# Optimization experiments

Hardware: AMD Instinct MI355X
Metric: run time of the kernel (lower is better)

## Reference

```python
import jax, jax.numpy as jnp
import numpy as np


def setup_inputs() -> dict:
    key = jax.random.key(0)
    k1, k2 = jax.random.split(key)
    flow = jax.random.normal(k1, (4, 2, 256, 256), dtype=jnp.float32)   # [B,2,H,W] per-pixel flow over dt
    spike = jax.random.uniform(k2, (4, 64, 256, 256), dtype=jnp.float32)  # [B,C,H,W] spike voxel grid
    return {"flow": flow, "spike": spike}


def _splat(vals, xn, yn, H, W):
    """Forward bilinear splat of vals [H,W] to continuous coords (xn,yn) [H,W]."""
    x0 = jnp.floor(xn)
    y0 = jnp.floor(yn)
    wx = xn - x0  # fractional weights (differentiable w.r.t. flow)
    wy = yn - y0
    x0i = x0.astype(jnp.int32)
    y0i = y0.astype(jnp.int32)
    out = jnp.zeros(H * W, dtype=vals.dtype)
    corners = (
        (0, 0, (1.0 - wx) * (1.0 - wy)),
        (1, 0, wx * (1.0 - wy)),
        (0, 1, (1.0 - wx) * wy),
        (1, 1, wx * wy),
    )
    for dx, dy, w in corners:
        xi = x0i + dx
        yi = y0i + dy
        valid = (xi >= 0) & (xi < W) & (yi >= 0) & (yi < H)
        idx = jnp.clip(yi, 0, H - 1) * W + jnp.clip(xi, 0, W - 1)
        out = out.at[idx.ravel()].add(jnp.where(valid, w * vals, 0.0).ravel())
    return out.reshape(H, W)


def spike_warp_mid(spike, flow, dt):
    """Warp each time bin c by flow * (c - mid)/dt toward the middle timestamp (bilinear splat)."""
    B, C, H, W = spike.shape
    mid = (C - 1) / 2.0
    yy, xx = jnp.meshgrid(jnp.arange(H, dtype=spike.dtype),
                          jnp.arange(W, dtype=spike.dtype), indexing='ij')
    s = (jnp.arange(C, dtype=spike.dtype) - mid) / jnp.asarray(dt, spike.dtype)  # [C]
    u = flow[:, 0][:, None]  # [B,1,H,W]
    v = flow[:, 1][:, None]
    xn = xx + u * s[None, :, None, None]  # [B,C,H,W]
    yn = yy + v * s[None, :, None, None]
    splat_bc = jax.vmap(jax.vmap(lambda va, xa, ya: _splat(va, xa, ya, H, W)))
    return splat_bc(spike, xn, yn)  # [B,C,H,W]


def reference(flow, spike):
    B, C, H, W = spike.shape
    spike_warped = spike_warp_mid(spike, flow, dt=64)
    # Faithful to original: sum over BATCH dim inside per-batch loop (same each iter),
    # so loss = (B * -var) / B = -var(spike_image) with unbiased variance.
    spike_image = jnp.sum(spike_warped, axis=0)  # [C,H,W]
    loss = -jnp.var(spike_image - jnp.mean(spike_image), ddof=1)
    return loss
```

## Files before the change

### kernel.cpp

```cpp
#include <hip/hip_runtime.h>

typedef float f2 __attribute__((ext_vector_type(2)));

constexpr int B = 4, C = 64, H = 256, W = 256;
constexpr int HW = H * W;
constexpr long long N_TOT = (long long)C * HW;

constexpr int TS = 16;
constexpr int R = 4;
constexpr int SW = 24;
constexpr int SAREA = SW * SW;
constexpr int NBLK = 256 * 8;

__global__ __launch_bounds__(256) void fused_kernel(
    const float* __restrict__ flow,
    const float* __restrict__ spike,
    double* __restrict__ partials) {
  __shared__ f2 uv[SAREA];
  __shared__ f2 spk[SAREA * 4];
  __shared__ float wmx[4], wmy[4];
  __shared__ double red[8];

  const int bid = blockIdx.x;
  const int tile = bid & 255;
  const int j = bid >> 8;
  const int tx0 = (tile & 15) * TS;
  const int ty0 = (tile >> 4) * TS;
  const int tid = threadIdx.x;
  const int qx = tid & 15, qy = tid >> 4;
  const int wave = tid >> 6;

  f2 smv[4];
  float smag3;
#pragma unroll
  for (int t = 0; t < 4; ++t) {
    float sm = ((float)(4 * j + t) + 0.5f) * (1.0f / 64.0f);
    smv[t] = f2{-sm, sm};
    if (t == 3) smag3 = sm;
  }
  const int cn0 = 31 - 4 * j;
  const int cp0 = 32 + 4 * j;

  f2 acc2[4];
#pragma unroll
  for (int t = 0; t < 4; ++t) acc2[t] = f2{0.f, 0.f};

  bool c_act[3], c_val[3];
  int c_apos[3], c_gp[3];
#pragma unroll
  for (int k = 0; k < 3; ++k) {
    int pos = tid + 256 * k;
    c_act[k] = pos < SAREA;
    int row = pos / SW;
    int col = pos - row * SW;
    c_apos[k] = pos;
    int gy = ty0 + row - R, gx = tx0 + col - R;
    c_val[k] = c_act[k] & ((unsigned)gy < (unsigned)H) & ((unsigned)gx < (unsigned)W);
    c_gp[k] = gy * W + gx;
  }

  float p_u[3], p_v[3];
  float4 p_a[3], p_b[3];

  auto prefetch = [&](int b) {
    const float* fu = flow + (size_t)b * 2 * HW;
    const float* fv = fu + HW;
    const float* spb = spike + (size_t)b * C * HW;
#pragma unroll
    for (int k = 0; k < 3; ++k) {
      float u = 0.f, v = 0.f;
      float4 a = {0.f, 0.f, 0.f, 0.f};
      float4 d = {0.f, 0.f, 0.f, 0.f};
      if (c_val[k]) {
        int gp = c_gp[k];
        u = fu[gp];
        v = fv[gp];
        a.x = spb[(size_t)cn0 * HW + gp];
        a.y = spb[(size_t)(cn0 - 1) * HW + gp];
        a.z = spb[(size_t)(cn0 - 2) * HW + gp];
        a.w = spb[(size_t)(cn0 - 3) * HW + gp];
        d.x = spb[(size_t)cp0 * HW + gp];
        d.y = spb[(size_t)(cp0 + 1) * HW + gp];
        d.z = spb[(size_t)(cp0 + 2) * HW + gp];
        d.w = spb[(size_t)(cp0 + 3) * HW + gp];
      }
      p_u[k] = u; p_v[k] = v; p_a[k] = a; p_b[k] = d;
    }
  };

  prefetch(0);

  const int qpos = (qy + R) * SW + (qx + R);

  for (int b = 0; b < B; ++b) {
    float mu = 0.f, mv = 0.f;
#pragma unroll
    for (int k = 0; k < 3; ++k) {
      if (c_act[k]) {
        int ap = c_apos[k];
        uv[ap] = f2{p_u[k], p_v[k]};
        f2* sp = &spk[ap * 4];
        sp[0] = f2{p_a[k].x, p_b[k].x};
        sp[1] = f2{p_a[k].y, p_b[k].y};
        sp[2] = f2{p_a[k].z, p_b[k].z};
        sp[3] = f2{p_a[k].w, p_b[k].w};
        mu = fmaxf(mu, fabsf(p_u[k]));
        mv = fmaxf(mv, fabsf(p_v[k]));
      }
    }
    for (int off = 32; off > 0; off >>= 1) {
      mu = fmaxf(mu, __shfl_down(mu, off, 64));
      mv = fmaxf(mv, __shfl_down(mv, off, 64));
    }
    if ((tid & 63) == 0) { wmx[wave] = mu; wmy[wave] = mv; }
    __syncthreads();
    float bu = fmaxf(fmaxf(wmx[0], wmx[1]), fmaxf(wmx[2], wmx[3]));
    float bv = fmaxf(fmaxf(wmy[0], wmy[1]), fmaxf(wmy[2], wmy[3]));
    int rx = min((int)(1.0f + bu * smag3), R);
    int ry = min((int)(1.0f + bv * smag3), R);

    if (b + 1 < B) prefetch(b + 1);

    for (int dy = -ry; dy <= ry; ++dy) {
      const f2 fdy2 = (float)dy;
      for (int dx = -rx; dx <= rx; ++dx) {
        const int pp = qpos + dy * SW + dx;
        f2 u2 = uv[pp];
        const f2* vp = &spk[pp * 4];
        const f2 fdx2 = (float)dx;
        const f2 ux = f2{u2.x, u2.x};
        const f2 vy = f2{u2.y, u2.y};
#pragma unroll
        for (int t = 0; t < 4; ++t) {
          f2 ax = __builtin_elementwise_fma(ux, smv[t], fdx2);
          f2 ay = __builtin_elementwise_fma(vy, smv[t], fdy2);
          f2 tx = __builtin_elementwise_max(1.0f - __builtin_elementwise_abs(ax), f2{0.f, 0.f});
          f2 ty = __builtin_elementwise_max(1.0f - __builtin_elementwise_abs(ay), f2{0.f, 0.f});
          acc2[t] = __builtin_elementwise_fma(tx * ty, vp[t], acc2[t]);
        }
      }
    }
    __syncthreads();
  }

  double ls = 0.0, lq = 0.0;
#pragma unroll
  for (int t = 0; t < 4; ++t) {
    double a = (double)acc2[t].x, b2 = (double)acc2[t].y;
    ls += a + b2;
    lq += a * a + b2 * b2;
  }
  for (int off = 32; off > 0; off >>= 1) {
    ls += __shfl_down(ls, off, 64);
    lq += __shfl_down(lq, off, 64);
  }
  if ((tid & 63) == 0) { red[wave * 2] = ls; red[wave * 2 + 1] = lq; }
  __syncthreads();
  if (tid == 0) {
    partials[2 * bid] = red[0] + red[2] + red[4] + red[6];
    partials[2 * bid + 1] = red[1] + red[3] + red[5] + red[7];
  }
}

__global__ __launch_bounds__(256) void finalize_kernel(
    const double* __restrict__ partials, float* __restrict__ out) {
  double s = 0.0, q = 0.0;
  for (int i = threadIdx.x; i < NBLK; i += 256) {
    s += partials[2 * i];
    q += partials[2 * i + 1];
  }
  for (int off = 32; off > 0; off >>= 1) {
    s += __shfl_down(s, off, 64);
    q += __shfl_down(q, off, 64);
  }
  __shared__ double ss[4], qq[4];
  int lane = threadIdx.x & 63;
  int wave = threadIdx.x >> 6;
  if (lane == 0) { ss[wave] = s; qq[wave] = q; }
  __syncthreads();
  if (threadIdx.x == 0) {
    double sum = ss[0] + ss[1] + ss[2] + ss[3];
    double sq = qq[0] + qq[1] + qq[2] + qq[3];
    double n = (double)N_TOT;
    double var = (sq - sum * sum / n) / (n - 1.0);
    out[0] = (float)(-var);
  }
}

extern "C" void kernel_launch(void* const* d_in, const int* in_sizes, int n_in,
                              void* d_out, int out_size, void* d_ws, size_t ws_size,
                              hipStream_t stream) {
  const float* flow = (const float*)d_in[0];
  const float* spike = (const float*)d_in[1];
  float* out = (float*)d_out;
  double* partials = (double*)d_ws;

  fused_kernel<<<dim3(NBLK), dim3(256), 0, stream>>>(flow, spike, partials);
  finalize_kernel<<<1, dim3(256), 0, stream>>>(partials, out);
}
```

Baseline: 156.3 us.

## Split splat into 3x3 gather plus atomic scatter overflow for large displacements

Each time bin's radius now depends on its displacement. Sources whose displacement magnitude is below 1 pixel are handled by a fixed 3x3 gather over an 18x18 inner tile. Larger displacements are scattered via LDS atomics into per-channel overflow planes, with out-of-tile targets dropped into sentinel columns and rows. The halo load shrinks per block index j, and the per-batch max-reduction barrier is removed. The cost is LDS atomics, whose contention rises with the fraction of large displacements, plus extra LDS for the overflow planes.

After: 148.6 us. 1.05x faster.

```diff
diff --git a/kernel.cpp b/kernel.cpp
--- a/kernel.cpp
+++ b/kernel.cpp
@@ -1,24 +1,28 @@
 #include <hip/hip_runtime.h>
 
 typedef float f2 __attribute__((ext_vector_type(2)));
+typedef float f4v __attribute__((ext_vector_type(4)));
 
 constexpr int B = 4, C = 64, H = 256, W = 256;
 constexpr int HW = H * W;
 constexpr long long N_TOT = (long long)C * HW;
 
 constexpr int TS = 16;
-constexpr int R = 4;
-constexpr int SW = 24;
-constexpr int SAREA = SW * SW;
+constexpr int INW = 18;
+constexpr int INA = INW * INW;
+constexpr int OVW = 19;
+constexpr int OVH = 18;
+constexpr int OVA = OVH * OVW;
 constexpr int NBLK = 256 * 8;
 
 __global__ __launch_bounds__(256) void fused_kernel(
     const float* __restrict__ flow,
     const float* __restrict__ spike,
     double* __restrict__ partials) {
-  __shared__ f2 uv[SAREA];
-  __shared__ f2 spk[SAREA * 4];
-  __shared__ float wmx[4], wmy[4];
+  __shared__ __align__(16) f4v spkA[INA];
+  __shared__ __align__(16) f4v spkB[INA];
+  __shared__ f2 uv[INA];
+  __shared__ __align__(16) float ovf[8 * OVA];
   __shared__ double red[8];
 
   const int bid = blockIdx.x;
@@ -30,42 +34,53 @@
   const int qx = tid & 15, qy = tid >> 4;
   const int wave = tid >> 6;
 
+  {
+    f4v z = {0.f, 0.f, 0.f, 0.f};
+    f4v* ov4 = (f4v*)ovf;
+    for (int i = tid; i < (8 * OVA) / 4; i += 256) ov4[i] = z;
+  }
+
   f2 smv[4];
-  float smag3;
+  float sm[4];
 #pragma unroll
   for (int t = 0; t < 4; ++t) {
-    float sm = ((float)(4 * j + t) + 0.5f) * (1.0f / 64.0f);
-    smv[t] = f2{-sm, sm};
-    if (t == 3) smag3 = sm;
+    float s = ((float)(4 * j + t) + 0.5f) * (1.0f / 64.0f);
+    sm[t] = s;
+    smv[t] = f2{-s, s};
   }
   const int cn0 = 31 - 4 * j;
   const int cp0 = 32 + 4 * j;
-
-  f2 acc2[4];
-#pragma unroll
-  for (int t = 0; t < 4; ++t) acc2[t] = f2{0.f, 0.f};
-
-  bool c_act[3], c_val[3];
-  int c_apos[3], c_gp[3];
+  const int Rj = (j >> 1) + 1;
+  const int SWj = TS + 2 * Rj;
+  const int SAj = SWj * SWj;
+
+  bool c_act[3], c_val[3], c_inn[3];
+  int c_gp[3], c_ip[3];
+  float c_px[3], c_py[3];
 #pragma unroll
   for (int k = 0; k < 3; ++k) {
     int pos = tid + 256 * k;
-    c_act[k] = pos < SAREA;
-    int row = pos / SW;
-    int col = pos - row * SW;
-    c_apos[k] = pos;
-    int gy = ty0 + row - R, gx = tx0 + col - R;
-    c_val[k] = c_act[k] & ((unsigned)gy < (unsigned)H) & ((unsigned)gx < (unsigned)W);
+    bool act = pos < SAj;
+    int row = act ? pos / SWj : 0;
+    int col = pos - row * SWj;
+    int relx = col - Rj, rely = row - Rj;
+    int gy = ty0 + rely, gx = tx0 + relx;
+    c_act[k] = act;
+    c_val[k] = act & ((unsigned)gy < (unsigned)H) & ((unsigned)gx < (unsigned)W);
     c_gp[k] = gy * W + gx;
+    c_inn[k] = act & (relx >= -1) & (relx <= 16) & (rely >= -1) & (rely <= 16);
+    c_ip[k] = (rely + 1) * INW + (relx + 1);
+    c_px[k] = (float)relx;
+    c_py[k] = (float)rely;
   }
 
   float p_u[3], p_v[3];
   float4 p_a[3], p_b[3];
 
-  auto prefetch = [&](int b) {
-    const float* fu = flow + (size_t)b * 2 * HW;
+  auto prefetch = [&](int bb) {
+    const float* fu = flow + (size_t)bb * 2 * HW;
     const float* fv = fu + HW;
-    const float* spb = spike + (size_t)b * C * HW;
+    const float* spb = spike + (size_t)bb * C * HW;
 #pragma unroll
     for (int k = 0; k < 3; ++k) {
       float u = 0.f, v = 0.f;
@@ -89,58 +104,103 @@
   };
 
   prefetch(0);
-
-  const int qpos = (qy + R) * SW + (qx + R);
-
-  for (int b = 0; b < B; ++b) {
-    float mu = 0.f, mv = 0.f;
+  __syncthreads();
+
+  const int qip = (qy + 1) * INW + (qx + 1);
+  f2 acc2[4];
+#pragma unroll
+  for (int t = 0; t < 4; ++t) acc2[t] = f2{0.f, 0.f};
+
+  for (int bb = 0; bb < B; ++bb) {
 #pragma unroll
     for (int k = 0; k < 3; ++k) {
-      if (c_act[k]) {
-        int ap = c_apos[k];
-        uv[ap] = f2{p_u[k], p_v[k]};
-        f2* sp = &spk[ap * 4];
-        sp[0] = f2{p_a[k].x, p_b[k].x};
-        sp[1] = f2{p_a[k].y, p_b[k].y};
-        sp[2] = f2{p_a[k].z, p_b[k].z};
-        sp[3] = f2{p_a[k].w, p_b[k].w};
-        mu = fmaxf(mu, fabsf(p_u[k]));
-        mv = fmaxf(mv, fabsf(p_v[k]));
+      if (!c_act[k]) continue;
+      float u = p_u[k], v = p_v[k];
+      float4 a = p_a[k], d = p_b[k];
+      float es = fmaxf(fabsf(u), fabsf(v));
+      bool ev0 = es * sm[0] >= 1.0f;
+      bool ev1 = es * sm[1] >= 1.0f;
+      bool ev2 = es * sm[2] >= 1.0f;
+      bool ev3 = es * sm[3] >= 1.0f;
+      if (c_inn[k]) {
+        int ip = c_ip[k];
+        uv[ip] = f2{u, v};
+        spkA[ip] = f4v{ev0 ? 0.f : a.x, ev0 ? 0.f : d.x,
+                       ev1 ? 0.f : a.y, ev1 ? 0.f : d.y};
+        spkB[ip] = f4v{ev2 ? 0.f : a.z, ev2 ? 0.f : d.z,
+                       ev3 ? 0.f : a.w, ev3 ? 0.f : d.w};
+      }
+      if (__any(ev3)) {
+        const f2 u2 = f2{u, u}, v2 = f2{v, v};
+        const f2 px2 = f2{c_px[k], c_px[k]}, py2 = f2{c_py[k], c_py[k]};
+        const float av[4] = {a.x, a.y, a.z, a.w};
+        const float bv[4] = {d.x, d.y, d.z, d.w};
+#pragma unroll
+        for (int t = 0; t < 4; ++t) {
+          bool ev = es * sm[t] >= 1.0f;
+          if (ev) {
+            f2 xn = __builtin_elementwise_fma(u2, smv[t], px2);
+            f2 yn = __builtin_elementwise_fma(v2, smv[t], py2);
+#pragma unroll
+            for (int h = 0; h < 2; ++h) {
+              float x = xn[h], y = yn[h];
+              float val = h ? bv[t] : av[t];
+              float fx = floorf(x), fy = floorf(y);
+              float f = x - fx, g = y - fy;
+              int X0 = (int)fx, Y0 = (int)fy;
+              int ix0 = ((unsigned)X0 < 16u) ? X0 + 1 : 17;
+              int ix1 = ((unsigned)(X0 + 1) < 16u) ? X0 + 2 : 18;
+              int iy0 = ((unsigned)Y0 < 16u) ? Y0 + 1 : 17;
+              int iy1 = ((unsigned)(Y0 + 1) < 16u) ? Y0 + 2 : 17;
+              float* pl = &ovf[(2 * t + h) * OVA];
+              float w1 = f * val, w0 = val - w1;
+              float g1 = g, g0 = 1.0f - g;
+              atomicAdd(pl + iy0 * OVW + ix0, w0 * g0);
+              atomicAdd(pl + iy0 * OVW + ix1, w1 * g0);
+              atomicAdd(pl + iy1 * OVW + ix0, w0 * g1);
+              atomicAdd(pl + iy1 * OVW + ix1, w1 * g1);
+            }
+          }
+        }
       }
     }
-    for (int off = 32; off > 0; off >>= 1) {
-      mu = fmaxf(mu, __shfl_down(mu, off, 64));
-      mv = fmaxf(mv, __shfl_down(mv, off, 64));
-    }
-    if ((tid & 63) == 0) { wmx[wave] = mu; wmy[wave] = mv; }
     __syncthreads();
-    float bu = fmaxf(fmaxf(wmx[0], wmx[1]), fmaxf(wmx[2], wmx[3]));
-    float bv = fmaxf(fmaxf(wmy[0], wmy[1]), fmaxf(wmy[2], wmy[3]));
-    int rx = min((int)(1.0f + bu * smag3), R);
-    int ry = min((int)(1.0f + bv * smag3), R);
-
-    if (b + 1 < B) prefetch(b + 1);
-
-    for (int dy = -ry; dy <= ry; ++dy) {
-      const f2 fdy2 = (float)dy;
-      for (int dx = -rx; dx <= rx; ++dx) {
-        const int pp = qpos + dy * SW + dx;
-        f2 u2 = uv[pp];
-        const f2* vp = &spk[pp * 4];
+    if (bb + 1 < B) prefetch(bb + 1);
+
+#pragma unroll
+    for (int dy = -1; dy <= 1; ++dy) {
+#pragma unroll
+      for (int dx = -1; dx <= 1; ++dx) {
+        const int ip = qip + dy * INW + dx;
+        const f2 u2v = uv[ip];
+        const f4v A = spkA[ip];
+        const f4v Bv = spkB[ip];
+        const f2 ux = f2{u2v.x, u2v.x};
+        const f2 vy = f2{u2v.y, u2v.y};
         const f2 fdx2 = (float)dx;
-        const f2 ux = f2{u2.x, u2.x};
-        const f2 vy = f2{u2.y, u2.y};
+        const f2 fdy2 = (float)dy;
+        const f2 vals[4] = {f2{A[0], A[1]}, f2{A[2], A[3]},
+                            f2{Bv[0], Bv[1]}, f2{Bv[2], Bv[3]}};
 #pragma unroll
         for (int t = 0; t < 4; ++t) {
           f2 ax = __builtin_elementwise_fma(ux, smv[t], fdx2);
           f2 ay = __builtin_elementwise_fma(vy, smv[t], fdy2);
-          f2 tx = __builtin_elementwise_max(1.0f - __builtin_elementwise_abs(ax), f2{0.f, 0.f});
-          f2 ty = __builtin_elementwise_max(1.0f - __builtin_elementwise_abs(ay), f2{0.f, 0.f});
-          acc2[t] = __builtin_elementwise_fma(tx * ty, vp[t], acc2[t]);
+          f2 tx, ty;
+          tx[0] = __builtin_amdgcn_fmed3f(1.0f - fabsf(ax[0]), 0.f, 1.f);
+          tx[1] = __builtin_amdgcn_fmed3f(1.0f - fabsf(ax[1]), 0.f, 1.f);
+          ty[0] = __builtin_amdgcn_fmed3f(1.0f - fabsf(ay[0]), 0.f, 1.f);
+          ty[1] = __builtin_amdgcn_fmed3f(1.0f - fabsf(ay[1]), 0.f, 1.f);
+          acc2[t] = __builtin_elementwise_fma(tx * ty, vals[t], acc2[t]);
         }
       }
     }
     __syncthreads();
+  }
+
+  const int oip = (qy + 1) * OVW + (qx + 1);
+#pragma unroll
+  for (int t = 0; t < 4; ++t) {
+    acc2[t] += f2{ovf[(2 * t) * OVA + oip], ovf[(2 * t + 1) * OVA + oip]};
   }
 
   double ls = 0.0, lq = 0.0;
```
